# Optimization experiments

Measured on AMD Instinct MI355X. Metric: run time of the kernel, lower is better.

## Reference

```python
import jax, jax.numpy as jnp
import numpy as np

DIM = 384
HEADS = 12
CUBE = (4, 7, 7)
N = CUBE[0] * CUBE[1] * CUBE[2]  # 196
HIDDEN = 4 * DIM
BW = 256  # num_windows * batch
EPS = 1e-5


def _relative_position_index():
    c, h, w = CUBE
    coords = np.stack(np.meshgrid(np.arange(c), np.arange(h), np.arange(w), indexing='ij'))  # [3,c,h,w]
    flat = coords.reshape(3, -1)  # [3, N]
    rel = flat[:, :, None] - flat[:, None, :]  # [3, N, N]
    rel = rel.transpose(1, 2, 0).copy()
    rel[:, :, 0] += c - 1
    rel[:, :, 1] += h - 1
    rel[:, :, 2] += w - 1
    rel[:, :, 1] *= 2 * w - 1
    rel[:, :, 0] *= (2 * h - 1) * (2 * w - 1)
    return rel.sum(-1).astype(np.int32)  # [N, N]


def setup_inputs() -> dict:
    key = jax.random.key(0)
    ks = jax.random.split(key, 16)
    s = 0.02
    table_rows = (2 * CUBE[0] - 1) * (2 * CUBE[1] - 1) * (2 * CUBE[2] - 1)
    return {
        'x': jax.random.normal(ks[0], (BW, N, DIM), jnp.float32),
        'norm1_w': jnp.ones((DIM,), jnp.float32),
        'norm1_b': jnp.zeros((DIM,), jnp.float32),
        'qkv_w': jax.random.normal(ks[1], (DIM, 3 * DIM), jnp.float32) * s,
        'qkv_b': jnp.zeros((3 * DIM,), jnp.float32),
        'proj_w': jax.random.normal(ks[2], (DIM, DIM), jnp.float32) * s,
        'proj_b': jnp.zeros((DIM,), jnp.float32),
        'rpb_table': jax.random.normal(ks[3], (table_rows, HEADS), jnp.float32) * s,
        'norm2_w': jnp.ones((DIM,), jnp.float32),
        'norm2_b': jnp.zeros((DIM,), jnp.float32),
        'fc1_w': jax.random.normal(ks[4], (DIM, HIDDEN), jnp.float32) * s,
        'fc1_b': jnp.zeros((HIDDEN,), jnp.float32),
        'fc2_w': jax.random.normal(ks[5], (HIDDEN, DIM), jnp.float32) * s,
        'fc2_b': jnp.zeros((DIM,), jnp.float32),
        'rpi': jnp.asarray(_relative_position_index()),
    }


def _layernorm(x, w, b):
    mu = jnp.mean(x, axis=-1, keepdims=True)
    var = jnp.mean(jnp.square(x - mu), axis=-1, keepdims=True)
    return (x - mu) * jax.lax.rsqrt(var + EPS) * w + b


def reference(x, norm1_w, norm1_b, qkv_w, qkv_b, proj_w, proj_b, rpb_table,
              norm2_w, norm2_b, fc1_w, fc1_b, fc2_w, fc2_b, rpi):
    B_, n, C = x.shape
    hd = C // HEADS
    scale = hd ** (-0.5)

    # --- attention branch ---
    h = _layernorm(x, norm1_w, norm1_b)
    qkv = (h @ qkv_w + qkv_b).reshape(B_, n, 3, HEADS, hd)
    q, k, v = qkv[:, :, 0], qkv[:, :, 1], qkv[:, :, 2]  # [B_, n, H, hd]
    attn = jnp.einsum('bqhd,bkhd->bhqk', q * scale, k)
    bias = rpb_table[rpi]                 # [n, n, H]
    attn = attn + jnp.transpose(bias, (2, 0, 1))[None]
    attn = jax.nn.softmax(attn, axis=-1)
    out = jnp.einsum('bhqk,bkhd->bqhd', attn, v).reshape(B_, n, C)
    out = out @ proj_w + proj_b
    x = x + out

    # --- MLP branch ---
    h = _layernorm(x, norm2_w, norm2_b)
    h = jax.nn.gelu(h @ fc1_w + fc1_b, approximate=False)
    h = h @ fc2_w + fc2_b
    return x + h
```

## Files before the change

kernel.cpp:

```cpp
#include <hip/hip_runtime.h>
#include <hip/hip_bf16.h>
#include <math.h>

#define NDIM 384
#define NHEADS 12
#define NTOK 196
#define NBATCH 256
#define M_TOK (NBATCH * NTOK)
#define NHID 1536
#define THREE_DIM 1152
#define HD 32
#define EPSV 1e-5f
#define BH_STRIDE 7168
#define BPAD 224

typedef __hip_bfloat16 bf16;
typedef __attribute__((ext_vector_type(8))) short short8;
typedef __attribute__((ext_vector_type(4))) short short4v;
typedef __attribute__((ext_vector_type(4))) float f32x4;

__device__ __forceinline__ void gload_lds16(const void* g, void* l) {
  __builtin_amdgcn_global_load_lds((const __attribute__((address_space(1))) void*)g,
                                   (__attribute__((address_space(3))) void*)l, 16, 0, 0);
}

__global__ void k_transpose_bf16(const float* __restrict__ src, bf16* __restrict__ dst,
                                 int K, int N) {
  int idx = blockIdx.x * 256 + threadIdx.x;
  if (idx >= K * N) return;
  int k = idx / N, n = idx - k * N;
  dst[n * K + k] = __float2bfloat16(src[idx]);
}

__global__ void k_build_bias(const float* __restrict__ table, const int* __restrict__ rpi,
                             float* __restrict__ bias_pad) {
  int idx = blockIdx.x * 256 + threadIdx.x;
  if (idx >= NHEADS * BPAD * BPAD) return;
  int h = idx / (BPAD * BPAD);
  int rem = idx - h * (BPAD * BPAD);
  int r = rem / BPAD, c = rem - r * BPAD;
  float v;
  if (c >= NTOK) {
    v = -1e30f;
  } else {
    int rr = r < NTOK ? r : NTOK - 1;
    v = table[rpi[rr * NTOK + c] * NHEADS + h];
  }
  bias_pad[idx] = v;
}

__global__ __launch_bounds__(256) void k_layernorm(const float* __restrict__ x,
                                                   const float* __restrict__ w,
                                                   const float* __restrict__ b,
                                                   bf16* __restrict__ out) {
  int token = blockIdx.x * 4 + (threadIdx.x >> 6);
  int lane = threadIdx.x & 63;
  const float* xr = x + (size_t)token * NDIM;
  float v[6];
  float s = 0.f;
#pragma unroll
  for (int i = 0; i < 6; ++i) { v[i] = xr[lane + i * 64]; s += v[i]; }
#pragma unroll
  for (int off = 32; off >= 1; off >>= 1) s += __shfl_xor(s, off);
  float mu = s * (1.f / NDIM);
  float s2 = 0.f;
#pragma unroll
  for (int i = 0; i < 6; ++i) { float d = v[i] - mu; s2 += d * d; }
#pragma unroll
  for (int off = 32; off >= 1; off >>= 1) s2 += __shfl_xor(s2, off);
  float r = rsqrtf(s2 * (1.f / NDIM) + EPSV);
  bf16* orow = out + (size_t)token * NDIM;
#pragma unroll
  for (int i = 0; i < 6; ++i) {
    int c = lane + i * 64;
    orow[c] = __float2bfloat16((v[i] - mu) * r * w[c] + b[c]);
  }
}

template <int EPI>
__global__ __launch_bounds__(256) void k_gemm_bt(const bf16* __restrict__ A,
                                                 const bf16* __restrict__ Bt,
                                                 const float* __restrict__ bias,
                                                 const float* __restrict__ resid,
                                                 void* __restrict__ Cout,
                                                 bf16* __restrict__ pq,
                                                 bf16* __restrict__ pk,
                                                 bf16* __restrict__ pv,
                                                 int Nn, int K, int nbx) {
  __shared__ __align__(16) bf16 As[2][4096];
  __shared__ __align__(16) bf16 Bs[2][4096];
  const int tid = threadIdx.x;
  const int wave = tid >> 6, lane = tid & 63;
  const int lo = lane & 15, hi = lane >> 4;
  const int wm = wave >> 1, wn = wave & 1;

  const int nwg = gridDim.x;
  const int swz = (blockIdx.x & 7) * (nwg >> 3) + (blockIdx.x >> 3);
  const int m0 = (swz / nbx) * 128, n0 = (swz % nbx) * 128;

  f32x4 acc[4][4];
#pragma unroll
  for (int i = 0; i < 4; ++i)
#pragma unroll
    for (int j = 0; j < 4; ++j) acc[i][j] = (f32x4){0.f, 0.f, 0.f, 0.f};

  const int row0 = tid >> 2, sw0 = (tid & 3) ^ ((row0 >> 1) & 3);
  const int c1 = 256 + tid;
  const int row1 = c1 >> 2, sw1 = (c1 & 3) ^ ((row1 >> 1) & 3);
  const bf16* Arow0 = A + (size_t)(m0 + row0) * K + sw0 * 8;
  const bf16* Brow0 = Bt + (size_t)(n0 + row0) * K + sw0 * 8;
  const bf16* Arow1 = A + (size_t)(m0 + row1) * K + sw1 * 8;
  const bf16* Brow1 = Bt + (size_t)(n0 + row1) * K + sw1 * 8;

#define STAGE(ks, abuf, bbuf)                                   \
  {                                                             \
    int k0_ = (ks) << 5;                                        \
    gload_lds16(Arow0 + k0_, (abuf) + tid * 8);                 \
    gload_lds16(Brow0 + k0_, (bbuf) + tid * 8);                 \
    gload_lds16(Arow1 + k0_, (abuf) + (256 + tid) * 8);         \
    gload_lds16(Brow1 + k0_, (bbuf) + (256 + tid) * 8);         \
  }

  const int nk = K >> 5;
  STAGE(0, As[0], Bs[0]);
  __syncthreads();

  const int rsw = (lo >> 1) & 3;
  int cur = 0;
  for (int ks = 0; ks < nk; ++ks) {
    if (ks + 1 < nk) STAGE(ks + 1, As[cur ^ 1], Bs[cur ^ 1]);
    short8 af[4], bfr[4];
#pragma unroll
    for (int i = 0; i < 4; ++i) {
      af[i] = *(const short8*)(As[cur] + (wm * 64 + i * 16 + lo) * 32 + (hi ^ rsw) * 8);
      bfr[i] = *(const short8*)(Bs[cur] + (wn * 64 + i * 16 + lo) * 32 + (hi ^ rsw) * 8);
    }
#pragma unroll
    for (int i = 0; i < 4; ++i)
#pragma unroll
      for (int j = 0; j < 4; ++j)
        acc[i][j] = __builtin_amdgcn_mfma_f32_16x16x32_bf16(bfr[j], af[i], acc[i][j], 0, 0, 0);
    __syncthreads();
    cur ^= 1;
  }
#undef STAGE

  const float qscale = 0.17677669529663687f;
#pragma unroll
  for (int i = 0; i < 4; ++i) {
    int r = m0 + wm * 64 + i * 16 + lo;
#pragma unroll
    for (int j = 0; j < 4; ++j) {
      int cb0 = n0 + wn * 64 + j * 16 + hi * 4;
      f32x4 bv = *(const f32x4*)(bias + cb0);
      f32x4 v;
#pragma unroll
      for (int e = 0; e < 4; ++e) v[e] = acc[i][j][e] + bv[e];
      if (EPI == 3) {
        int d0 = cb0 & 31;
        int hseg = cb0 >> 5;
        int which = hseg / 12;
        int h = hseg - which * 12;
        int b = r / 196;
        int t = r - b * 196;
        size_t base = (size_t)(b * 12 + h) * BH_STRIDE;
        if (which == 2) {
#pragma unroll
          for (int e = 0; e < 4; ++e)
            pv[base + (d0 + e) * BPAD + t] = __float2bfloat16(v[e]);
        } else if (which == 1) {
          union { short4v s; bf16 x[4]; } pack;
#pragma unroll
          for (int e = 0; e < 4; ++e) pack.x[e] = __float2bfloat16(v[e]);
          *(short4v*)(pk + base + t * 32 + d0) = pack.s;
        } else {
          union { short4v s; bf16 x[4]; } pack;
#pragma unroll
          for (int e = 0; e < 4; ++e) pack.x[e] = __float2bfloat16(v[e] * qscale);
          *(short4v*)(pq + base + t * 32 + d0) = pack.s;
        }
      } else if (EPI == 2) {
        size_t idx = (size_t)r * Nn + cb0;
        f32x4 rs = *(const f32x4*)(resid + idx);
#pragma unroll
        for (int e = 0; e < 4; ++e) v[e] += rs[e];
        *(f32x4*)((float*)Cout + idx) = v;
      } else {
        if (EPI == 1) {
#pragma unroll
          for (int e = 0; e < 4; ++e) {
            float val = v[e];
            float t = val * val;
            float p = __builtin_fmaf(0.044715f * val, t, val);
            float E = __expf(1.5957691216057308f * p);
            float rr = __builtin_amdgcn_rcpf(E + 1.f);
            v[e] = val - val * rr;
          }
        }
        union { short4v s; bf16 x[4]; } pack;
#pragma unroll
        for (int e = 0; e < 4; ++e) pack.x[e] = __float2bfloat16(v[e]);
        size_t idx = (size_t)r * Nn + cb0;
        *(short4v*)((bf16*)Cout + idx) = pack.s;
      }
    }
  }
}

__global__ __launch_bounds__(256) void k_attn(const bf16* __restrict__ Qp,
                                              const bf16* __restrict__ Kp,
                                              const bf16* __restrict__ Vtp,
                                              const float* __restrict__ bias_pad,
                                              bf16* __restrict__ out) {
  __shared__ __align__(16) bf16 Ps[4][16][232];
  const int tid = threadIdx.x;
  const int wave = tid >> 6, lane = tid & 63;
  const int lo = lane & 15, hi = lane >> 4;
  const int nwg = gridDim.x;
  const int swz = (blockIdx.x & 7) * (nwg >> 3) + (blockIdx.x >> 3);
  const int unit = swz * 4 + wave;
  const int bh = unit / 13;
  const int qt = unit - bh * 13;
  const int h = bh % 12;
  const int b = bh / 12;
  const bf16* Qb = Qp + (size_t)bh * BH_STRIDE;
  const bf16* Kb = Kp + (size_t)bh * BH_STRIDE;
  const bf16* Vb = Vtp + (size_t)bh * BH_STRIDE;

  for (int i = lane; i < 256; i += 64)
    Ps[wave][i >> 4][208 + (i & 15)] = __float2bfloat16(0.f);

  short8 qf = *(const short8*)(Qb + (qt * 16 + lo) * 32 + hi * 8);

  f32x4 s[13];
  __builtin_amdgcn_s_setprio(1);
#pragma unroll
  for (int kt = 0; kt < 13; ++kt) {
    short8 kf = *(const short8*)(Kb + (kt * 16 + lo) * 32 + hi * 8);
    f32x4 z = {0.f, 0.f, 0.f, 0.f};
    s[kt] = __builtin_amdgcn_mfma_f32_16x16x32_bf16(qf, kf, z, 0, 0, 0);
  }
  __builtin_amdgcn_s_setprio(0);

#pragma unroll
  for (int e = 0; e < 4; ++e) {
    int qg = qt * 16 + hi * 4 + e;
    const float* brow = bias_pad + ((size_t)h * BPAD + qg) * BPAD;
    float mx = -1e30f;
#pragma unroll
    for (int kt = 0; kt < 13; ++kt) {
      float v = s[kt][e] + brow[kt * 16 + lo];
      s[kt][e] = v;
      mx = fmaxf(mx, v);
    }
#pragma unroll
    for (int off = 8; off >= 1; off >>= 1) mx = fmaxf(mx, __shfl_xor(mx, off));
    float sm = 0.f;
#pragma unroll
    for (int kt = 0; kt < 13; ++kt) {
      float pe = __expf(s[kt][e] - mx);
      s[kt][e] = pe;
      sm += pe;
    }
#pragma unroll
    for (int off = 8; off >= 1; off >>= 1) sm += __shfl_xor(sm, off);
    float inv = 1.f / sm;
#pragma unroll
    for (int kt = 0; kt < 13; ++kt) s[kt][e] *= inv;
  }

#pragma unroll
  for (int kt = 0; kt < 13; ++kt) {
#pragma unroll
    for (int e = 0; e < 4; ++e)
      Ps[wave][hi * 4 + e][kt * 16 + lo] = __float2bfloat16(s[kt][e]);
  }

  f32x4 o[2] = {{0.f, 0.f, 0.f, 0.f}, {0.f, 0.f, 0.f, 0.f}};
  __builtin_amdgcn_s_setprio(1);
#pragma unroll
  for (int c = 0; c < 7; ++c) {
    short8 pa = *(const short8*)(&Ps[wave][lo][c * 32 + hi * 8]);
#pragma unroll
    for (int n = 0; n < 2; ++n) {
      short8 vf = *(const short8*)(Vb + (n * 16 + lo) * BPAD + c * 32 + hi * 8);
      o[n] = __builtin_amdgcn_mfma_f32_16x16x32_bf16(pa, vf, o[n], 0, 0, 0);
    }
  }
  __builtin_amdgcn_s_setprio(0);

#pragma unroll
  for (int n = 0; n < 2; ++n) {
#pragma unroll
    for (int e = 0; e < 4; ++e) {
      int qg = qt * 16 + hi * 4 + e;
      if (qg < NTOK)
        out[(size_t)(b * NTOK + qg) * NDIM + h * HD + n * 16 + lo] = __float2bfloat16(o[n][e]);
    }
  }
}

extern "C" void kernel_launch(void* const* d_in, const int* in_sizes, int n_in,
                              void* d_out, int out_size, void* d_ws, size_t ws_size,
                              hipStream_t stream) {
  const float* x       = (const float*)d_in[0];
  const float* norm1_w = (const float*)d_in[1];
  const float* norm1_b = (const float*)d_in[2];
  const float* qkv_w   = (const float*)d_in[3];
  const float* qkv_b   = (const float*)d_in[4];
  const float* proj_w  = (const float*)d_in[5];
  const float* proj_b  = (const float*)d_in[6];
  const float* rpb     = (const float*)d_in[7];
  const float* norm2_w = (const float*)d_in[8];
  const float* norm2_b = (const float*)d_in[9];
  const float* fc1_w   = (const float*)d_in[10];
  const float* fc1_b   = (const float*)d_in[11];
  const float* fc2_w   = (const float*)d_in[12];
  const float* fc2_b   = (const float*)d_in[13];
  const int*   rpi     = (const int*)d_in[14];
  float* out = (float*)d_out;

  char* ws = (char*)d_ws;
  bf16* pad_q = (bf16*)ws;
  bf16* pad_k = (bf16*)(ws + 44040192);
  bf16* pad_v = (bf16*)(ws + 2 * 44040192);
  float* bias_pad = (float*)(ws + 3 * 44040192);
  bf16* mlp1 = (bf16*)ws;
  bf16* hbuf = (bf16*)(ws + 154140672);
  bf16* wqkv_t = (bf16*)(ws + 154140672 + 38535168);
  bf16* wproj_t = wqkv_t + 442368;
  bf16* wfc1_t = wproj_t + 147456;
  bf16* wfc2_t = wfc1_t + 589824;

  k_transpose_bf16<<<(442368 + 255) / 256, 256, 0, stream>>>(qkv_w, wqkv_t, 384, 1152);
  k_transpose_bf16<<<(147456 + 255) / 256, 256, 0, stream>>>(proj_w, wproj_t, 384, 384);
  k_transpose_bf16<<<(589824 + 255) / 256, 256, 0, stream>>>(fc1_w, wfc1_t, 384, 1536);
  k_transpose_bf16<<<(589824 + 255) / 256, 256, 0, stream>>>(fc2_w, wfc2_t, 1536, 384);
  k_build_bias<<<(NHEADS * BPAD * BPAD + 255) / 256, 256, 0, stream>>>(rpb, rpi, bias_pad);

  k_layernorm<<<M_TOK / 4, 256, 0, stream>>>(x, norm1_w, norm1_b, hbuf);
  k_gemm_bt<3><<<9 * 392, 256, 0, stream>>>(hbuf, wqkv_t, qkv_b, nullptr, nullptr,
                                            pad_q, pad_k, pad_v, 1152, 384, 9);
  k_attn<<<9984, 256, 0, stream>>>(pad_q, pad_k, pad_v, bias_pad, hbuf);
  k_gemm_bt<2><<<3 * 392, 256, 0, stream>>>(hbuf, wproj_t, proj_b, x, out,
                                            nullptr, nullptr, nullptr, 384, 384, 3);
  k_layernorm<<<M_TOK / 4, 256, 0, stream>>>(out, norm2_w, norm2_b, hbuf);
  k_gemm_bt<1><<<12 * 392, 256, 0, stream>>>(hbuf, wfc1_t, fc1_b, nullptr, mlp1,
                                             nullptr, nullptr, nullptr, 1536, 384, 12);
  k_gemm_bt<2><<<3 * 392, 256, 0, stream>>>(mlp1, wfc2_t, fc2_b, out, out,
                                            nullptr, nullptr, nullptr, 384, 1536, 3);
}
```

Baseline: 534.1 us.

## Add strip GEMM keeping full 64-row A tile in LDS for K=384 GEMMs

Adds a GEMM kernel in which each block loads an entire 64xK strip of A into swizzled LDS once. Each wave then sweeps 64-column output tiles, reading B fragments straight from global memory (cache-resident weights) with no double-buffered staging or per-k-step barriers. It replaces the tiled GEMM for the QKV, proj and fc1 GEMMs, and the shared epilogue is factored into a helper. In exchange, B loads come directly from global without LDS reuse, each wave works on only 64x64 tiles with no cross-wave B sharing, and the grid is much smaller (784 blocks), which may limit latency hiding.

```diff
diff --git a/kernel.cpp b/kernel.cpp
--- a/kernel.cpp
+++ b/kernel.cpp
@@ -74,6 +74,131 @@
   for (int i = 0; i < 6; ++i) {
     int c = lane + i * 64;
     orow[c] = __float2bfloat16((v[i] - mu) * r * w[c] + b[c]);
+  }
+}
+
+template <int EPI>
+__device__ __forceinline__ void gemm_epilogue(const f32x4 acc[4][4], int m0, int n0,
+                                              int lo, int hi,
+                                              const float* __restrict__ bias,
+                                              const float* __restrict__ resid,
+                                              void* __restrict__ Cout,
+                                              bf16* __restrict__ pq,
+                                              bf16* __restrict__ pk,
+                                              bf16* __restrict__ pv, int Nn) {
+  const float qscale = 0.17677669529663687f;
+#pragma unroll
+  for (int i = 0; i < 4; ++i) {
+    int r = m0 + i * 16 + lo;
+#pragma unroll
+    for (int j = 0; j < 4; ++j) {
+      int cb0 = n0 + j * 16 + hi * 4;
+      f32x4 bv = *(const f32x4*)(bias + cb0);
+      f32x4 v;
+#pragma unroll
+      for (int e = 0; e < 4; ++e) v[e] = acc[i][j][e] + bv[e];
+      if (EPI == 3) {
+        int d0 = cb0 & 31;
+        int hseg = cb0 >> 5;
+        int which = hseg / 12;
+        int h = hseg - which * 12;
+        int b = r / 196;
+        int t = r - b * 196;
+        size_t base = (size_t)(b * 12 + h) * BH_STRIDE;
+        if (which == 2) {
+#pragma unroll
+          for (int e = 0; e < 4; ++e)
+            pv[base + (d0 + e) * BPAD + t] = __float2bfloat16(v[e]);
+        } else if (which == 1) {
+          union { short4v s; bf16 x[4]; } pack;
+#pragma unroll
+          for (int e = 0; e < 4; ++e) pack.x[e] = __float2bfloat16(v[e]);
+          *(short4v*)(pk + base + t * 32 + d0) = pack.s;
+        } else {
+          union { short4v s; bf16 x[4]; } pack;
+#pragma unroll
+          for (int e = 0; e < 4; ++e) pack.x[e] = __float2bfloat16(v[e] * qscale);
+          *(short4v*)(pq + base + t * 32 + d0) = pack.s;
+        }
+      } else if (EPI == 2) {
+        size_t idx = (size_t)r * Nn + cb0;
+        f32x4 rs = *(const f32x4*)(resid + idx);
+#pragma unroll
+        for (int e = 0; e < 4; ++e) v[e] += rs[e];
+        *(f32x4*)((float*)Cout + idx) = v;
+      } else {
+        if (EPI == 1) {
+#pragma unroll
+          for (int e = 0; e < 4; ++e) {
+            float val = v[e];
+            float t = val * val;
+            float p = __builtin_fmaf(0.044715f * val, t, val);
+            float E = __expf(1.5957691216057308f * p);
+            float rr = __builtin_amdgcn_rcpf(E + 1.f);
+            v[e] = val - val * rr;
+          }
+        }
+        union { short4v s; bf16 x[4]; } pack;
+#pragma unroll
+        for (int e = 0; e < 4; ++e) pack.x[e] = __float2bfloat16(v[e]);
+        size_t idx = (size_t)r * Nn + cb0;
+        *(short4v*)((bf16*)Cout + idx) = pack.s;
+      }
+    }
+  }
+}
+
+template <int EPI, int NK, int NT>
+__global__ __launch_bounds__(256) void k_gemm_strip(const bf16* __restrict__ A,
+                                                    const bf16* __restrict__ Bt,
+                                                    const float* __restrict__ bias,
+                                                    const float* __restrict__ resid,
+                                                    void* __restrict__ Cout,
+                                                    bf16* __restrict__ pq,
+                                                    bf16* __restrict__ pk,
+                                                    bf16* __restrict__ pv,
+                                                    int Nn) {
+  constexpr int K = NK * 32;
+  constexpr int NCH = K / 8;
+  __shared__ __align__(16) bf16 As[64 * K];
+  const int tid = threadIdx.x;
+  const int wave = tid >> 6, lane = tid & 63;
+  const int lo = lane & 15, hi = lane >> 4;
+  const int m0 = blockIdx.x * 64;
+
+#pragma unroll
+  for (int u = 0; u < (64 * NCH) / 256; ++u) {
+    int c = u * 256 + tid;
+    int r = c / NCH, cc = c - r * NCH;
+    gload_lds16(A + (size_t)(m0 + r) * K + (cc ^ (r & 7)) * 8, As + c * 8);
+  }
+  __syncthreads();
+
+#pragma unroll 1
+  for (int wt = wave; wt < NT; wt += 4) {
+    const int n0 = wt * 64;
+    f32x4 acc[4][4];
+#pragma unroll
+    for (int i = 0; i < 4; ++i)
+#pragma unroll
+      for (int j = 0; j < 4; ++j) acc[i][j] = (f32x4){0.f, 0.f, 0.f, 0.f};
+
+#pragma unroll
+    for (int ks = 0; ks < NK; ++ks) {
+      short8 af[4], bfr[4];
+#pragma unroll
+      for (int i = 0; i < 4; ++i)
+        af[i] = *(const short8*)(As + (i * 16 + lo) * K + (((ks * 4 + hi) ^ (lo & 7)) * 8));
+#pragma unroll
+      for (int j = 0; j < 4; ++j)
+        bfr[j] = *(const short8*)(Bt + (size_t)(n0 + j * 16 + lo) * K + ks * 32 + hi * 8);
+#pragma unroll
+      for (int i = 0; i < 4; ++i)
+#pragma unroll
+        for (int j = 0; j < 4; ++j)
+          acc[i][j] = __builtin_amdgcn_mfma_f32_16x16x32_bf16(bfr[j], af[i], acc[i][j], 0, 0, 0);
+    }
+    gemm_epilogue<EPI>(acc, m0, n0, lo, hi, bias, resid, Cout, pq, pk, pv, Nn);
   }
 }
 
@@ -145,66 +270,8 @@
   }
 #undef STAGE
 
-  const float qscale = 0.17677669529663687f;
-#pragma unroll
-  for (int i = 0; i < 4; ++i) {
-    int r = m0 + wm * 64 + i * 16 + lo;
-#pragma unroll
-    for (int j = 0; j < 4; ++j) {
-      int cb0 = n0 + wn * 64 + j * 16 + hi * 4;
-      f32x4 bv = *(const f32x4*)(bias + cb0);
-      f32x4 v;
-#pragma unroll
-      for (int e = 0; e < 4; ++e) v[e] = acc[i][j][e] + bv[e];
-      if (EPI == 3) {
-        int d0 = cb0 & 31;
-        int hseg = cb0 >> 5;
-        int which = hseg / 12;
-        int h = hseg - which * 12;
-        int b = r / 196;
-        int t = r - b * 196;
-        size_t base = (size_t)(b * 12 + h) * BH_STRIDE;
-        if (which == 2) {
-#pragma unroll
-          for (int e = 0; e < 4; ++e)
-            pv[base + (d0 + e) * BPAD + t] = __float2bfloat16(v[e]);
-        } else if (which == 1) {
-          union { short4v s; bf16 x[4]; } pack;
-#pragma unroll
-          for (int e = 0; e < 4; ++e) pack.x[e] = __float2bfloat16(v[e]);
-          *(short4v*)(pk + base + t * 32 + d0) = pack.s;
-        } else {
-          union { short4v s; bf16 x[4]; } pack;
-#pragma unroll
-          for (int e = 0; e < 4; ++e) pack.x[e] = __float2bfloat16(v[e] * qscale);
-          *(short4v*)(pq + base + t * 32 + d0) = pack.s;
-        }
-      } else if (EPI == 2) {
-        size_t idx = (size_t)r * Nn + cb0;
-        f32x4 rs = *(const f32x4*)(resid + idx);
-#pragma unroll
-        for (int e = 0; e < 4; ++e) v[e] += rs[e];
-        *(f32x4*)((float*)Cout + idx) = v;
-      } else {
-        if (EPI == 1) {
-#pragma unroll
-          for (int e = 0; e < 4; ++e) {
-            float val = v[e];
-            float t = val * val;
-            float p = __builtin_fmaf(0.044715f * val, t, val);
-            float E = __expf(1.5957691216057308f * p);
-            float rr = __builtin_amdgcn_rcpf(E + 1.f);
-            v[e] = val - val * rr;
-          }
-        }
-        union { short4v s; bf16 x[4]; } pack;
-#pragma unroll
-        for (int e = 0; e < 4; ++e) pack.x[e] = __float2bfloat16(v[e]);
-        size_t idx = (size_t)r * Nn + cb0;
-        *(short4v*)((bf16*)Cout + idx) = pack.s;
-      }
-    }
-  }
+  gemm_epilogue<EPI>(acc, m0 + wm * 64, n0 + wn * 64, lo, hi, bias, resid, Cout,
+                     pq, pk, pv, Nn);
 }
 
 __global__ __launch_bounds__(256) void k_attn(const bf16* __restrict__ Qp,
@@ -339,14 +406,14 @@
   k_build_bias<<<(NHEADS * BPAD * BPAD + 255) / 256, 256, 0, stream>>>(rpb, rpi, bias_pad);
 
   k_layernorm<<<M_TOK / 4, 256, 0, stream>>>(x, norm1_w, norm1_b, hbuf);
-  k_gemm_bt<3><<<9 * 392, 256, 0, stream>>>(hbuf, wqkv_t, qkv_b, nullptr, nullptr,
-                                            pad_q, pad_k, pad_v, 1152, 384, 9);
+  k_gemm_strip<3, 12, 18><<<M_TOK / 64, 256, 0, stream>>>(hbuf, wqkv_t, qkv_b, nullptr,
+                                                          nullptr, pad_q, pad_k, pad_v, 1152);
   k_attn<<<9984, 256, 0, stream>>>(pad_q, pad_k, pad_v, bias_pad, hbuf);
-  k_gemm_bt<2><<<3 * 392, 256, 0, stream>>>(hbuf, wproj_t, proj_b, x, out,
-                                            nullptr, nullptr, nullptr, 384, 384, 3);
+  k_gemm_strip<2, 12, 6><<<M_TOK / 64, 256, 0, stream>>>(hbuf, wproj_t, proj_b, x, out,
+                                                         nullptr, nullptr, nullptr, 384);
   k_layernorm<<<M_TOK / 4, 256, 0, stream>>>(out, norm2_w, norm2_b, hbuf);
-  k_gemm_bt<1><<<12 * 392, 256, 0, stream>>>(hbuf, wfc1_t, fc1_b, nullptr, mlp1,
-                                             nullptr, nullptr, nullptr, 1536, 384, 12);
+  k_gemm_strip<1, 12, 24><<<M_TOK / 64, 256, 0, stream>>>(hbuf, wfc1_t, fc1_b, nullptr, mlp1,
+                                                          nullptr, nullptr, nullptr, 1536);
   k_gemm_bt<2><<<3 * 392, 256, 0, stream>>>(mlp1, wfc2_t, fc2_b, out, out,
                                             nullptr, nullptr, nullptr, 384, 1536, 3);
 }
```

New measurement: 760.8 us. +42.5%, slower.
